# Kernel optimization log

Hardware: AMD Instinct MI355X
Metric: run time of the kernel (lower is better)

The kernel has to match this reference:

```python
import jax, jax.numpy as jnp
import numpy as np

B, S, DIM = 32, 1, 4096
HQ, HKV, HD = 32, 8, 128
MAX_SEQ = 2048
START_POS = 2047


def _apply_rope(t, cos, sin):
    # t: [B, S, H, HD]; cos/sin: [S, HD//2]; interleaved complex rotation (Llama style)
    b, s, h, d = t.shape
    t = t.reshape(b, s, h, d // 2, 2)
    t0, t1 = t[..., 0], t[..., 1]
    c = cos[None, :, None, :]
    sn = sin[None, :, None, :]
    out = jnp.stack([t0 * c - t1 * sn, t0 * sn + t1 * c], axis=-1)
    return out.reshape(b, s, h, d)


def setup_inputs() -> dict:
    key = jax.random.key(0)
    ks = jax.random.split(key, 8)
    w_scale = 0.02
    x = jax.random.normal(ks[0], (B, S, DIM), dtype=jnp.float32)
    wq = jax.random.normal(ks[1], (HQ * HD, DIM), dtype=jnp.float32) * w_scale
    wk = jax.random.normal(ks[2], (HKV * HD, DIM), dtype=jnp.float32) * w_scale
    wv = jax.random.normal(ks[3], (HKV * HD, DIM), dtype=jnp.float32) * w_scale
    wo = jax.random.normal(ks[4], (HQ * HD, DIM), dtype=jnp.float32).T * w_scale
    wo = jnp.asarray(wo)  # [DIM, HQ*HD] as torch Linear weight [out,in]
    cache_k = jax.random.normal(ks[5], (B, MAX_SEQ, HKV, HD), dtype=jnp.float32)
    cache_v = jax.random.normal(ks[6], (B, MAX_SEQ, HKV, HD), dtype=jnp.float32)
    # rotary frequencies for the current position(s)
    inv_freq = 1.0 / (10000.0 ** (np.arange(0, HD, 2, dtype=np.float32) / HD))  # [HD//2]
    pos = np.arange(START_POS, START_POS + S, dtype=np.float32)[:, None]  # [S,1]
    ang = pos * inv_freq[None, :]
    freqs_cos = jnp.asarray(np.cos(ang), dtype=jnp.float32)
    freqs_sin = jnp.asarray(np.sin(ang), dtype=jnp.float32)
    return {"x": x, "wq": wq, "wk": wk, "wv": wv, "wo": wo,
            "cache_k": cache_k, "cache_v": cache_v,
            "freqs_cos": freqs_cos, "freqs_sin": freqs_sin,
            "start_pos": START_POS}


def reference(x, wq, wk, wv, wo, cache_k, cache_v, freqs_cos, freqs_sin, start_pos):
    b, s, dim = x.shape
    hd = 2 * freqs_cos.shape[-1]
    hq = wq.shape[0] // hd
    hkv = wk.shape[0] // hd
    n_rep = hq // hkv

    # QKV projections (torch Linear: y = x @ W.T)
    xq = (x @ wq.T).reshape(b, s, hq, hd)
    xk = (x @ wk.T).reshape(b, s, hkv, hd)
    xv = (x @ wv.T).reshape(b, s, hkv, hd)

    # RoPE on q and k
    xq = _apply_rope(xq, freqs_cos, freqs_sin)
    xk = _apply_rope(xk, freqs_cos, freqs_sin)

    # KV cache update at start_pos (static python int -> static slicing)
    ck = jax.lax.dynamic_update_slice(cache_k, xk, (0, start_pos, 0, 0))
    cv = jax.lax.dynamic_update_slice(cache_v, xv, (0, start_pos, 0, 0))
    t = start_pos + s
    keys = ck[:, :t]    # [B, T, HKV, HD]
    values = cv[:, :t]  # [B, T, HKV, HD]

    # Grouped attention without materializing repeated KV (repeat_kv fused into einsum)
    q = xq.reshape(b, s, hkv, n_rep, hd)
    scores = jnp.einsum('bsgrd,btgd->bgrst', q, keys) / jnp.sqrt(jnp.asarray(hd, x.dtype))
    attn = jax.nn.softmax(scores, axis=-1)  # decode step: attends to full history, no mask
    out = jnp.einsum('bgrst,btgd->bsgrd', attn, values).reshape(b, s, hq * hd)
    return out @ wo.T  # [B, S, DIM]
```

## Files before the change

### kernel.cpp

```cpp
#include <hip/hip_runtime.h>
#include <hip/hip_bf16.h>

typedef float vf4 __attribute__((ext_vector_type(4)));

#define B_    32
#define DIM_  4096
#define TSEQ  2048
#define LASTT 2047
#define NCH   8
#define CHUNK 256
#define SCL   0.08838834764831845f
#define KS    16
#define KCH   256
#define ROWS1 6144
#define ROWS4 4096

__device__ __forceinline__ float dotv(vf4 a, vf4 b) {
    return fmaf(a[0], b[0], fmaf(a[1], b[1], fmaf(a[2], b[2], a[3] * b[3])));
}

__device__ __forceinline__ void gemm_tile_part(
    const float* __restrict__ W, const float* __restrict__ X,
    float* __restrict__ part, int rloc_base, int grow_base,
    int kb0, int kc, int rowsTot) {
    __shared__ __align__(16) vf4 wS[128][17];
    __shared__ __align__(16) vf4 xS[16][33];
    const int tid = threadIdx.x;
    const int rg = tid >> 3, bg = tid & 7;
    const int sr4 = tid >> 4, swf = tid & 15;
    const int sb = tid >> 3, sxf = tid & 7;
    float c[4][4] = {};

    for (int tile = 0; tile < 4; ++tile) {
        const int kb4 = (kb0 + tile * 64) >> 2;
        #pragma unroll
        for (int jj = 0; jj < 8; ++jj) {
            const int row = sr4 + 16 * jj;
            wS[row][swf] =
                ((const vf4*)(W + (size_t)(rloc_base + row) * DIM_))[kb4 + swf];
        }
        #pragma unroll
        for (int jj = 0; jj < 2; ++jj) {
            const int f4i = sxf + 8 * jj;
            xS[f4i][sb] = ((const vf4*)(X + (size_t)sb * DIM_))[kb4 + f4i];
        }
        __syncthreads();
        #pragma unroll
        for (int k4 = 0; k4 < 16; ++k4) {
            const vf4 w0 = wS[rg      ][k4];
            const vf4 w1 = wS[rg + 32 ][k4];
            const vf4 w2 = wS[rg + 64 ][k4];
            const vf4 w3 = wS[rg + 96 ][k4];
            const vf4 x0 = xS[k4][bg     ];
            const vf4 x1 = xS[k4][bg + 8 ];
            const vf4 x2 = xS[k4][bg + 16];
            const vf4 x3 = xS[k4][bg + 24];
            #pragma unroll
            for (int cm = 0; cm < 4; ++cm) {
                c[0][0] = fmaf(w0[cm], x0[cm], c[0][0]);
                c[0][1] = fmaf(w0[cm], x1[cm], c[0][1]);
                c[0][2] = fmaf(w0[cm], x2[cm], c[0][2]);
                c[0][3] = fmaf(w0[cm], x3[cm], c[0][3]);
                c[1][0] = fmaf(w1[cm], x0[cm], c[1][0]);
                c[1][1] = fmaf(w1[cm], x1[cm], c[1][1]);
                c[1][2] = fmaf(w1[cm], x2[cm], c[1][2]);
                c[1][3] = fmaf(w1[cm], x3[cm], c[1][3]);
                c[2][0] = fmaf(w2[cm], x0[cm], c[2][0]);
                c[2][1] = fmaf(w2[cm], x1[cm], c[2][1]);
                c[2][2] = fmaf(w2[cm], x2[cm], c[2][2]);
                c[2][3] = fmaf(w2[cm], x3[cm], c[2][3]);
                c[3][0] = fmaf(w3[cm], x0[cm], c[3][0]);
                c[3][1] = fmaf(w3[cm], x1[cm], c[3][1]);
                c[3][2] = fmaf(w3[cm], x2[cm], c[3][2]);
                c[3][3] = fmaf(w3[cm], x3[cm], c[3][3]);
            }
        }
        __syncthreads();
    }
    float* pb = part + (size_t)kc * rowsTot * 32;
    #pragma unroll
    for (int i = 0; i < 4; ++i)
        #pragma unroll
        for (int j = 0; j < 4; ++j)
            pb[(size_t)(grow_base + rg + 32 * i) * 32 + bg + 8 * j] = c[i][j];
}

__global__ __launch_bounds__(256) void k1_qkv(
    const float* __restrict__ x,  const float* __restrict__ wq,
    const float* __restrict__ wk, const float* __restrict__ wv,
    float* __restrict__ part) {
    const int rb = blockIdx.x >> 4, kc = blockIdx.x & 15;
    const int rbase = rb * 128;
    const float* W; int rloc;
    if (rbase < 4096)      { W = wq; rloc = rbase; }
    else if (rbase < 5120) { W = wk; rloc = rbase - 4096; }
    else                   { W = wv; rloc = rbase - 5120; }
    gemm_tile_part(W, x, part, rloc, rbase, kc * KCH, kc, ROWS1);
}

__global__ __launch_bounds__(256) void k1b_comb(
    const float* __restrict__ part, const float* __restrict__ fcos,
    const float* __restrict__ fsin, float* __restrict__ q_ws,
    float* __restrict__ k_ws, float* __restrict__ v_ws) {
    const int tid = threadIdx.x;
    const int b = tid & 31;
    const int row0 = (blockIdx.x * 8 + (tid >> 5)) * 2;
    float e = 0.f, o = 0.f;
    #pragma unroll
    for (int kc = 0; kc < 16; ++kc) {
        const float* pb = part + (size_t)kc * (ROWS1 * 32);
        e += pb[(size_t)row0 * 32 + b];
        o += pb[(size_t)(row0 + 1) * 32 + b];
    }
    if (row0 < 5120) {
        const int d = row0 & 127;
        const float cj = fcos[d >> 1], sj = fsin[d >> 1];
        const float re = e * cj - o * sj;
        const float ro = e * sj + o * cj;
        if (row0 < 4096) {
            q_ws[(size_t)b * 4096 + row0]     = re * SCL;
            q_ws[(size_t)b * 4096 + row0 + 1] = ro * SCL;
        } else {
            k_ws[(size_t)b * 1024 + row0 - 4096] = re;
            k_ws[(size_t)b * 1024 + row0 - 4095] = ro;
        }
    } else {
        v_ws[(size_t)b * 1024 + row0 - 5120] = e;
        v_ws[(size_t)b * 1024 + row0 - 5119] = o;
    }
}

__global__ __launch_bounds__(256) void k2_attn(
    const float* __restrict__ q_ws, const float* __restrict__ k_ws,
    const float* __restrict__ v_ws, const float* __restrict__ cK,
    const float* __restrict__ cV,   float* __restrict__ cws) {
    __shared__ __align__(16) float p_lds[4][260];
    __shared__ __align__(16) float pacc[4][4][128];
    __shared__ float wred[4][4];
    __shared__ float wsum[4][4];
    const int blk = blockIdx.x;
    const int b = blk >> 6, g = (blk >> 3) & 7, c = blk & 7;
    const int tid = threadIdx.x, wave = tid >> 6, lane = tid & 63;
    const int tbase = c * CHUNK + wave * 64;
    const int s = lane & 7, pown = lane >> 3;

    const vf4* qb4 = (const vf4*)(q_ws + ((size_t)b * 32 + g * 4) * 128);
    vf4 q4[4][4];
    #pragma unroll
    for (int r = 0; r < 4; ++r)
        #pragma unroll
        for (int j = 0; j < 4; ++j)
            q4[r][j] = qb4[r * 32 + j * 8 + s];

    const vf4* kwsrow = (const vf4*)(k_ws + ((size_t)b * 8 + g) * 128);
    const vf4* vwsrow = (const vf4*)(v_ws + ((size_t)b * 8 + g) * 128);

    vf4 kb[4];
    {
        const int t = tbase + pown;
        const vf4* kr = (t == LASTT) ? kwsrow
            : (const vf4*)(cK + (((size_t)b * TSEQ + t) * 8 + g) * 128);
        #pragma unroll
        for (int j = 0; j < 4; ++j)
            kb[j] = __builtin_nontemporal_load(&kr[j * 8 + s]);
    }
    #pragma unroll
    for (int pg = 0; pg < 8; ++pg) {
        vf4 kn[4];
        if (pg < 7) {
            const int t = tbase + (pg + 1) * 8 + pown;
            const vf4* kr = (t == LASTT) ? kwsrow
                : (const vf4*)(cK + (((size_t)b * TSEQ + t) * 8 + g) * 128);
            #pragma unroll
            for (int j = 0; j < 4; ++j)
                kn[j] = __builtin_nontemporal_load(&kr[j * 8 + s]);
        }
        float a0 = 0.f, a1 = 0.f, a2 = 0.f, a3 = 0.f;
        #pragma unroll
        for (int j = 0; j < 4; ++j) {
            a0 += dotv(q4[0][j], kb[j]);
            a1 += dotv(q4[1][j], kb[j]);
            a2 += dotv(q4[2][j], kb[j]);
            a3 += dotv(q4[3][j], kb[j]);
        }
        #pragma unroll
        for (int m = 4; m >= 1; m >>= 1) {
            a0 += __shfl_xor(a0, m); a1 += __shfl_xor(a1, m);
            a2 += __shfl_xor(a2, m); a3 += __shfl_xor(a3, m);
        }
        const int idx = wave * 64 + pg * 8 + pown;
        if (s == 0) p_lds[0][idx] = a0;
        if (s == 1) p_lds[1][idx] = a1;
        if (s == 2) p_lds[2][idx] = a2;
        if (s == 3) p_lds[3][idx] = a3;
        #pragma unroll
        for (int j = 0; j < 4; ++j) kb[j] = kn[j];
    }

    float sc[4];
    #pragma unroll
    for (int r = 0; r < 4; ++r) sc[r] = p_lds[r][wave * 64 + lane];
    #pragma unroll
    for (int r = 0; r < 4; ++r) {
        float m = sc[r];
        #pragma unroll
        for (int msk = 32; msk >= 1; msk >>= 1) m = fmaxf(m, __shfl_xor(m, msk));
        if (lane == 0) wred[wave][r] = m;
    }
    __syncthreads();
    float M[4], S[4];
    #pragma unroll
    for (int r = 0; r < 4; ++r)
        M[r] = fmaxf(fmaxf(wred[0][r], wred[1][r]), fmaxf(wred[2][r], wred[3][r]));
    #pragma unroll
    for (int r = 0; r < 4; ++r) {
        const float p = __expf(sc[r] - M[r]);
        p_lds[r][wave * 64 + lane] = p;
        float su = p;
        #pragma unroll
        for (int msk = 32; msk >= 1; msk >>= 1) su += __shfl_xor(su, msk);
        if (lane == 0) wsum[wave][r] = su;
    }
    __syncthreads();
    #pragma unroll
    for (int r = 0; r < 4; ++r)
        S[r] = wsum[0][r] + wsum[1][r] + wsum[2][r] + wsum[3][r];

    const int h = lane >> 5, col = lane & 31;
    float a[4][4] = {};
    #pragma unroll
    for (int tt = 0; tt < 8; ++tt) {
        vf4 vv[4];
        #pragma unroll
        for (int u = 0; u < 4; ++u) {
            const int t = tbase + tt * 8 + u * 2 + h;
            const vf4* vp = (t == LASTT) ? vwsrow
                : (const vf4*)(cV + (((size_t)b * TSEQ + t) * 8 + g) * 128);
            vv[u] = __builtin_nontemporal_load(&vp[col]);
        }
        #pragma unroll
        for (int u = 0; u < 4; ++u) {
            #pragma unroll
            for (int r = 0; r < 4; ++r) {
                const float pr = p_lds[r][wave * 64 + tt * 8 + u * 2 + h];
                a[r][0] = fmaf(pr, vv[u][0], a[r][0]);
                a[r][1] = fmaf(pr, vv[u][1], a[r][1]);
                a[r][2] = fmaf(pr, vv[u][2], a[r][2]);
                a[r][3] = fmaf(pr, vv[u][3], a[r][3]);
            }
        }
    }
    #pragma unroll
    for (int r = 0; r < 4; ++r)
        #pragma unroll
        for (int j = 0; j < 4; ++j) a[r][j] += __shfl_xor(a[r][j], 32);
    if (lane < 32) {
        #pragma unroll
        for (int r = 0; r < 4; ++r) {
            vf4 v; v[0] = a[r][0]; v[1] = a[r][1]; v[2] = a[r][2]; v[3] = a[r][3];
            *(vf4*)&pacc[wave][r][col * 4] = v;
        }
    }
    __syncthreads();
    const size_t base = (size_t)blk * 520;
    for (int o = tid; o < 512; o += 256) {
        const int r = o >> 7, d = o & 127;
        cws[base + r * 130 + d] =
            pacc[0][r][d] + pacc[1][r][d] + pacc[2][r][d] + pacc[3][r][d];
    }
    if (tid == 0) {
        #pragma unroll
        for (int r = 0; r < 4; ++r) {
            cws[base + r * 130 + 128] = M[r];
            cws[base + r * 130 + 129] = S[r];
        }
    }
}

__global__ __launch_bounds__(256) void k3_comb(const float* __restrict__ cws,
                                               float* __restrict__ attn) {
    const int blk = blockIdx.x;
    const int b = blk >> 3, g = blk & 7;
    const int tid = threadIdx.x, r = tid >> 6, lane = tid & 63;
    const size_t base0 = (size_t)blk * 8 * 520 + r * 130;
    float mi[8], si[8];
    float Mg = -3.4e38f;
    #pragma unroll
    for (int ci = 0; ci < 8; ++ci) {
        mi[ci] = cws[base0 + (size_t)ci * 520 + 128];
        si[ci] = cws[base0 + (size_t)ci * 520 + 129];
        Mg = fmaxf(Mg, mi[ci]);
    }
    float w[8], Sg = 0.f;
    #pragma unroll
    for (int ci = 0; ci < 8; ++ci) {
        w[ci] = __expf(mi[ci] - Mg);
        Sg = fmaf(si[ci], w[ci], Sg);
    }
    const float inv = 1.f / Sg;
    #pragma unroll
    for (int dd = 0; dd < 2; ++dd) {
        const int d = lane + dd * 64;
        float o = 0.f;
        #pragma unroll
        for (int ci = 0; ci < 8; ++ci)
            o = fmaf(cws[base0 + (size_t)ci * 520 + d], w[ci], o);
        attn[((size_t)b * 32 + g * 4 + r) * 128 + d] = o * inv;
    }
}

__global__ __launch_bounds__(256) void k4_out(
    const float* __restrict__ attn, const float* __restrict__ wo,
    float* __restrict__ part) {
    const int rb = blockIdx.x >> 4, kc = blockIdx.x & 15;
    const int rbase = rb * 128;
    gemm_tile_part(wo, attn, part, rbase, rbase, kc * KCH, kc, ROWS4);
}

__global__ __launch_bounds__(256) void k4b_comb(const float* __restrict__ part,
                                                float* __restrict__ out) {
    const int tid = threadIdx.x;
    const int b = tid & 31;
    const int row = blockIdx.x * 8 + (tid >> 5);
    float acc = 0.f;
    #pragma unroll
    for (int kc = 0; kc < 16; ++kc)
        acc += part[(size_t)kc * (ROWS4 * 32) + (size_t)row * 32 + b];
    out[(size_t)b * 4096 + row] = acc;
}

extern "C" void kernel_launch(void* const* d_in, const int* in_sizes, int n_in,
                              void* d_out, int out_size, void* d_ws, size_t ws_size,
                              hipStream_t stream) {
    const float* x    = (const float*)d_in[0];
    const float* wq   = (const float*)d_in[1];
    const float* wk   = (const float*)d_in[2];
    const float* wv   = (const float*)d_in[3];
    const float* wo   = (const float*)d_in[4];
    const float* cK   = (const float*)d_in[5];
    const float* cV   = (const float*)d_in[6];
    const float* fcos = (const float*)d_in[7];
    const float* fsin = (const float*)d_in[8];
    float* ws   = (float*)d_ws;
    float* A    = ws;
    float* q_ws = ws + 3145728;
    float* k_ws = ws + 3276800;
    float* v_ws = ws + 3309568;
    float* attn = ws + 3342336;
    float* out  = (float*)d_out;

    hipLaunchKernelGGL(k1_qkv,   dim3(768),  dim3(256), 0, stream,
                       x, wq, wk, wv, A);
    hipLaunchKernelGGL(k1b_comb, dim3(384),  dim3(256), 0, stream,
                       A, fcos, fsin, q_ws, k_ws, v_ws);
    hipLaunchKernelGGL(k2_attn,  dim3(2048), dim3(256), 0, stream,
                       q_ws, k_ws, v_ws, cK, cV, A);
    hipLaunchKernelGGL(k3_comb,  dim3(256),  dim3(256), 0, stream, A, attn);
    hipLaunchKernelGGL(k4_out,   dim3(512),  dim3(256), 0, stream, attn, wo, A);
    hipLaunchKernelGGL(k4b_comb, dim3(512),  dim3(256), 0, stream, A, out);
}
```

Baseline: 160.7 us.

## Replace split-K partial buffers with atomic reductions and prefetch V in attention

The QKV and output GEMMs now accumulate their split-K partial sums straight into zeroed destination buffers with float atomicAdd. RoPE moves into the GEMM epilogue, using a lane shuffle to pair even and odd rows. This removes the two combine kernels and the round trip of the partial buffer through memory, at the cost of two memsets, atomic contention and non-deterministic summation order. The attention kernel also software-pipelines the V-cache loads one step ahead, and weight loads become nontemporal.

```diff
diff --git a/kernel.cpp b/kernel.cpp
--- a/kernel.cpp
+++ b/kernel.cpp
@@ -10,34 +10,29 @@
 #define NCH   8
 #define CHUNK 256
 #define SCL   0.08838834764831845f
-#define KS    16
 #define KCH   256
-#define ROWS1 6144
-#define ROWS4 4096
 
 __device__ __forceinline__ float dotv(vf4 a, vf4 b) {
     return fmaf(a[0], b[0], fmaf(a[1], b[1], fmaf(a[2], b[2], a[3] * b[3])));
 }
 
-__device__ __forceinline__ void gemm_tile_part(
+__device__ __forceinline__ void gemm_tile(
     const float* __restrict__ W, const float* __restrict__ X,
-    float* __restrict__ part, int rloc_base, int grow_base,
-    int kb0, int kc, int rowsTot) {
+    int kb0, float c[4][4]) {
     __shared__ __align__(16) vf4 wS[128][17];
     __shared__ __align__(16) vf4 xS[16][33];
     const int tid = threadIdx.x;
     const int rg = tid >> 3, bg = tid & 7;
     const int sr4 = tid >> 4, swf = tid & 15;
     const int sb = tid >> 3, sxf = tid & 7;
-    float c[4][4] = {};
 
     for (int tile = 0; tile < 4; ++tile) {
         const int kb4 = (kb0 + tile * 64) >> 2;
         #pragma unroll
         for (int jj = 0; jj < 8; ++jj) {
             const int row = sr4 + 16 * jj;
-            wS[row][swf] =
-                ((const vf4*)(W + (size_t)(rloc_base + row) * DIM_))[kb4 + swf];
+            wS[row][swf] = __builtin_nontemporal_load(
+                ((const vf4*)(W + (size_t)row * DIM_)) + kb4 + swf);
         }
         #pragma unroll
         for (int jj = 0; jj < 2; ++jj) {
@@ -77,56 +72,47 @@
         }
         __syncthreads();
     }
-    float* pb = part + (size_t)kc * rowsTot * 32;
-    #pragma unroll
-    for (int i = 0; i < 4; ++i)
-        #pragma unroll
-        for (int j = 0; j < 4; ++j)
-            pb[(size_t)(grow_base + rg + 32 * i) * 32 + bg + 8 * j] = c[i][j];
 }
 
 __global__ __launch_bounds__(256) void k1_qkv(
     const float* __restrict__ x,  const float* __restrict__ wq,
     const float* __restrict__ wk, const float* __restrict__ wv,
-    float* __restrict__ part) {
+    const float* __restrict__ fcos, const float* __restrict__ fsin,
+    float* __restrict__ q_ws, float* __restrict__ k_ws, float* __restrict__ v_ws) {
     const int rb = blockIdx.x >> 4, kc = blockIdx.x & 15;
     const int rbase = rb * 128;
-    const float* W; int rloc;
-    if (rbase < 4096)      { W = wq; rloc = rbase; }
-    else if (rbase < 5120) { W = wk; rloc = rbase - 4096; }
-    else                   { W = wv; rloc = rbase - 5120; }
-    gemm_tile_part(W, x, part, rloc, rbase, kc * KCH, kc, ROWS1);
-}
-
-__global__ __launch_bounds__(256) void k1b_comb(
-    const float* __restrict__ part, const float* __restrict__ fcos,
-    const float* __restrict__ fsin, float* __restrict__ q_ws,
-    float* __restrict__ k_ws, float* __restrict__ v_ws) {
+    const float* W; int rloc, kind;
+    if (rbase < 4096)      { W = wq; rloc = rbase;        kind = 0; }
+    else if (rbase < 5120) { W = wk; rloc = rbase - 4096; kind = 1; }
+    else                   { W = wv; rloc = rbase - 5120; kind = 2; }
+    float c[4][4] = {};
+    gemm_tile(W + (size_t)rloc * DIM_, x, kc * KCH, c);
+
     const int tid = threadIdx.x;
-    const int b = tid & 31;
-    const int row0 = (blockIdx.x * 8 + (tid >> 5)) * 2;
-    float e = 0.f, o = 0.f;
-    #pragma unroll
-    for (int kc = 0; kc < 16; ++kc) {
-        const float* pb = part + (size_t)kc * (ROWS1 * 32);
-        e += pb[(size_t)row0 * 32 + b];
-        o += pb[(size_t)(row0 + 1) * 32 + b];
-    }
-    if (row0 < 5120) {
-        const int d = row0 & 127;
-        const float cj = fcos[d >> 1], sj = fsin[d >> 1];
-        const float re = e * cj - o * sj;
-        const float ro = e * sj + o * cj;
-        if (row0 < 4096) {
-            q_ws[(size_t)b * 4096 + row0]     = re * SCL;
-            q_ws[(size_t)b * 4096 + row0 + 1] = ro * SCL;
-        } else {
-            k_ws[(size_t)b * 1024 + row0 - 4096] = re;
-            k_ws[(size_t)b * 1024 + row0 - 4095] = ro;
-        }
-    } else {
-        v_ws[(size_t)b * 1024 + row0 - 5120] = e;
-        v_ws[(size_t)b * 1024 + row0 - 5119] = o;
+    const int rg = tid >> 3, bg = tid & 7;
+    float* dst = (kind == 0) ? q_ws : (kind == 1 ? k_ws : v_ws);
+    const int stride = (kind == 0) ? 4096 : 1024;
+    #pragma unroll
+    for (int i = 0; i < 4; ++i) {
+        const int row = rloc + rg + 32 * i;
+        float vals[4];
+        #pragma unroll
+        for (int j = 0; j < 4; ++j) vals[j] = c[i][j];
+        if (kind <= 1) {
+            const int pi = (row & 126) >> 1;
+            const float cj = fcos[pi], sj = fsin[pi];
+            #pragma unroll
+            for (int j = 0; j < 4; ++j) {
+                const float partner = __shfl_xor(vals[j], 8);
+                float v = ((rg & 1) == 0) ? (vals[j] * cj - partner * sj)
+                                          : (partner * sj + vals[j] * cj);
+                if (kind == 0) v *= SCL;
+                vals[j] = v;
+            }
+        }
+        #pragma unroll
+        for (int j = 0; j < 4; ++j)
+            atomicAdd(&dst[(size_t)(bg + 8 * j) * stride + row], vals[j]);
     }
 }
 
@@ -197,6 +183,16 @@
         for (int j = 0; j < 4; ++j) kb[j] = kn[j];
     }
 
+    const int h = lane >> 5, col = lane & 31;
+    vf4 vb[4];
+    #pragma unroll
+    for (int u = 0; u < 4; ++u) {
+        const int t = tbase + u * 2 + h;
+        const vf4* vp = (t == LASTT) ? vwsrow
+            : (const vf4*)(cV + (((size_t)b * TSEQ + t) * 8 + g) * 128);
+        vb[u] = __builtin_nontemporal_load(&vp[col]);
+    }
+
     float sc[4];
     #pragma unroll
     for (int r = 0; r < 4; ++r) sc[r] = p_lds[r][wave * 64 + lane];
@@ -226,29 +222,32 @@
     for (int r = 0; r < 4; ++r)
         S[r] = wsum[0][r] + wsum[1][r] + wsum[2][r] + wsum[3][r];
 
-    const int h = lane >> 5, col = lane & 31;
     float a[4][4] = {};
     #pragma unroll
     for (int tt = 0; tt < 8; ++tt) {
-        vf4 vv[4];
-        #pragma unroll
-        for (int u = 0; u < 4; ++u) {
-            const int t = tbase + tt * 8 + u * 2 + h;
-            const vf4* vp = (t == LASTT) ? vwsrow
-                : (const vf4*)(cV + (((size_t)b * TSEQ + t) * 8 + g) * 128);
-            vv[u] = __builtin_nontemporal_load(&vp[col]);
+        vf4 vn[4];
+        if (tt < 7) {
+            #pragma unroll
+            for (int u = 0; u < 4; ++u) {
+                const int t = tbase + (tt + 1) * 8 + u * 2 + h;
+                const vf4* vp = (t == LASTT) ? vwsrow
+                    : (const vf4*)(cV + (((size_t)b * TSEQ + t) * 8 + g) * 128);
+                vn[u] = __builtin_nontemporal_load(&vp[col]);
+            }
         }
         #pragma unroll
         for (int u = 0; u < 4; ++u) {
             #pragma unroll
             for (int r = 0; r < 4; ++r) {
                 const float pr = p_lds[r][wave * 64 + tt * 8 + u * 2 + h];
-                a[r][0] = fmaf(pr, vv[u][0], a[r][0]);
-                a[r][1] = fmaf(pr, vv[u][1], a[r][1]);
-                a[r][2] = fmaf(pr, vv[u][2], a[r][2]);
-                a[r][3] = fmaf(pr, vv[u][3], a[r][3]);
+                a[r][0] = fmaf(pr, vb[u][0], a[r][0]);
+                a[r][1] = fmaf(pr, vb[u][1], a[r][1]);
+                a[r][2] = fmaf(pr, vb[u][2], a[r][2]);
+                a[r][3] = fmaf(pr, vb[u][3], a[r][3]);
             }
         }
+        #pragma unroll
+        for (int u = 0; u < 4; ++u) vb[u] = vn[u];
     }
     #pragma unroll
     for (int r = 0; r < 4; ++r)
@@ -311,22 +310,20 @@
 
 __global__ __launch_bounds__(256) void k4_out(
     const float* __restrict__ attn, const float* __restrict__ wo,
-    float* __restrict__ part) {
+    float* __restrict__ out) {
     const int rb = blockIdx.x >> 4, kc = blockIdx.x & 15;
     const int rbase = rb * 128;
-    gemm_tile_part(wo, attn, part, rbase, rbase, kc * KCH, kc, ROWS4);
-}
-
-__global__ __launch_bounds__(256) void k4b_comb(const float* __restrict__ part,
-                                                float* __restrict__ out) {
+    float c[4][4] = {};
+    gemm_tile(wo + (size_t)rbase * DIM_, attn, kc * KCH, c);
     const int tid = threadIdx.x;
-    const int b = tid & 31;
-    const int row = blockIdx.x * 8 + (tid >> 5);
-    float acc = 0.f;
-    #pragma unroll
-    for (int kc = 0; kc < 16; ++kc)
-        acc += part[(size_t)kc * (ROWS4 * 32) + (size_t)row * 32 + b];
-    out[(size_t)b * 4096 + row] = acc;
+    const int rg = tid >> 3, bg = tid & 7;
+    #pragma unroll
+    for (int i = 0; i < 4; ++i) {
+        const int row = rbase + rg + 32 * i;
+        #pragma unroll
+        for (int j = 0; j < 4; ++j)
+            atomicAdd(&out[(size_t)(bg + 8 * j) * 4096 + row], c[i][j]);
+    }
 }
 
 extern "C" void kernel_launch(void* const* d_in, const int* in_sizes, int n_in,
@@ -342,20 +339,19 @@
     const float* fcos = (const float*)d_in[7];
     const float* fsin = (const float*)d_in[8];
     float* ws   = (float*)d_ws;
-    float* A    = ws;
-    float* q_ws = ws + 3145728;
-    float* k_ws = ws + 3276800;
-    float* v_ws = ws + 3309568;
-    float* attn = ws + 3342336;
+    float* q_ws = ws;
+    float* k_ws = ws + 131072;
+    float* v_ws = ws + 163840;
+    float* cws  = ws + 196608;
+    float* attn = ws + 1261568;
     float* out  = (float*)d_out;
 
-    hipLaunchKernelGGL(k1_qkv,   dim3(768),  dim3(256), 0, stream,
-                       x, wq, wk, wv, A);
-    hipLaunchKernelGGL(k1b_comb, dim3(384),  dim3(256), 0, stream,
-                       A, fcos, fsin, q_ws, k_ws, v_ws);
-    hipLaunchKernelGGL(k2_attn,  dim3(2048), dim3(256), 0, stream,
-                       q_ws, k_ws, v_ws, cK, cV, A);
-    hipLaunchKernelGGL(k3_comb,  dim3(256),  dim3(256), 0, stream, A, attn);
-    hipLaunchKernelGGL(k4_out,   dim3(512),  dim3(256), 0, stream, attn, wo, A);
-    hipLaunchKernelGGL(k4b_comb, dim3(512),  dim3(256), 0, stream, A, out);
-}
+    hipMemsetAsync(q_ws, 0, 196608 * sizeof(float), stream);
+    hipMemsetAsync(out,  0, (size_t)out_size * sizeof(float), stream);
+    hipLaunchKernelGGL(k1_qkv,  dim3(768),  dim3(256), 0, stream,
+                       x, wq, wk, wv, fcos, fsin, q_ws, k_ws, v_ws);
+    hipLaunchKernelGGL(k2_attn, dim3(2048), dim3(256), 0, stream,
+                       q_ws, k_ws, v_ws, cK, cV, cws);
+    hipLaunchKernelGGL(k3_comb, dim3(256),  dim3(256), 0, stream, cws, attn);
+    hipLaunchKernelGGL(k4_out,  dim3(512),  dim3(256), 0, stream, attn, wo, out);
+}
```

Result: slower. 196.4 us (+22.2%).

## Split attention into single-wave 64-token chunks and pipeline V loads

Applied to the files above, without the earlier changes.

The attention kernel changes from 256-thread blocks over 256-token chunks to 64-thread, single-wave blocks over 64-token chunks (8192 blocks). This removes the cross-wave LDS reductions and most barriers, and each block writes its partial result directly. The PV loop now prefetches the next V row one step ahead, and the combine kernel merges 32 partials instead of 8, which means more workspace traffic. Weight tiles in the GEMM are also loaded with nontemporal hints.

```diff
diff --git a/kernel.cpp b/kernel.cpp
--- a/kernel.cpp
+++ b/kernel.cpp
@@ -7,10 +7,11 @@
 #define DIM_  4096
 #define TSEQ  2048
 #define LASTT 2047
-#define NCH   8
-#define CHUNK 256
+#define NCH   32
+#define CHUNK 64
+#define CSTR  528
+#define RSTR  132
 #define SCL   0.08838834764831845f
-#define KS    16
 #define KCH   256
 #define ROWS1 6144
 #define ROWS4 4096
@@ -36,8 +37,8 @@
         #pragma unroll
         for (int jj = 0; jj < 8; ++jj) {
             const int row = sr4 + 16 * jj;
-            wS[row][swf] =
-                ((const vf4*)(W + (size_t)(rloc_base + row) * DIM_))[kb4 + swf];
+            wS[row][swf] = __builtin_nontemporal_load(
+                ((const vf4*)(W + (size_t)(rloc_base + row) * DIM_)) + kb4 + swf);
         }
         #pragma unroll
         for (int jj = 0; jj < 2; ++jj) {
@@ -130,18 +131,15 @@
     }
 }
 
-__global__ __launch_bounds__(256) void k2_attn(
+__global__ __launch_bounds__(64) void k2_attn(
     const float* __restrict__ q_ws, const float* __restrict__ k_ws,
     const float* __restrict__ v_ws, const float* __restrict__ cK,
     const float* __restrict__ cV,   float* __restrict__ cws) {
-    __shared__ __align__(16) float p_lds[4][260];
-    __shared__ __align__(16) float pacc[4][4][128];
-    __shared__ float wred[4][4];
-    __shared__ float wsum[4][4];
+    __shared__ float p_lds[4][64];
     const int blk = blockIdx.x;
-    const int b = blk >> 6, g = (blk >> 3) & 7, c = blk & 7;
-    const int tid = threadIdx.x, wave = tid >> 6, lane = tid & 63;
-    const int tbase = c * CHUNK + wave * 64;
+    const int b = blk >> 8, g = (blk >> 5) & 7, c = blk & 31;
+    const int lane = threadIdx.x & 63;
+    const int tbase = c * CHUNK;
     const int s = lane & 7, pown = lane >> 3;
 
     const vf4* qb4 = (const vf4*)(q_ws + ((size_t)b * 32 + g * 4) * 128);
@@ -188,7 +186,7 @@
             a0 += __shfl_xor(a0, m); a1 += __shfl_xor(a1, m);
             a2 += __shfl_xor(a2, m); a3 += __shfl_xor(a3, m);
         }
-        const int idx = wave * 64 + pg * 8 + pown;
+        const int idx = pg * 8 + pown;
         if (s == 0) p_lds[0][idx] = a0;
         if (s == 1) p_lds[1][idx] = a1;
         if (s == 2) p_lds[2][idx] = a2;
@@ -196,83 +194,73 @@
         #pragma unroll
         for (int j = 0; j < 4; ++j) kb[j] = kn[j];
     }
-
-    float sc[4];
-    #pragma unroll
-    for (int r = 0; r < 4; ++r) sc[r] = p_lds[r][wave * 64 + lane];
+    __syncthreads();
+
+    const int h = lane >> 5, col = lane & 31;
+    vf4 vb;
+    {
+        const int t = tbase + h;
+        const vf4* vp = (t == LASTT) ? vwsrow
+            : (const vf4*)(cV + (((size_t)b * TSEQ + t) * 8 + g) * 128);
+        vb = __builtin_nontemporal_load(&vp[col]);
+    }
+
+    float sc[4], M[4], S[4];
+    #pragma unroll
+    for (int r = 0; r < 4; ++r) sc[r] = p_lds[r][lane];
     #pragma unroll
     for (int r = 0; r < 4; ++r) {
         float m = sc[r];
         #pragma unroll
         for (int msk = 32; msk >= 1; msk >>= 1) m = fmaxf(m, __shfl_xor(m, msk));
-        if (lane == 0) wred[wave][r] = m;
+        M[r] = m;
+        const float p = __expf(sc[r] - m);
+        p_lds[r][lane] = p;
+        float su = p;
+        #pragma unroll
+        for (int msk = 32; msk >= 1; msk >>= 1) su += __shfl_xor(su, msk);
+        S[r] = su;
     }
     __syncthreads();
-    float M[4], S[4];
-    #pragma unroll
-    for (int r = 0; r < 4; ++r)
-        M[r] = fmaxf(fmaxf(wred[0][r], wred[1][r]), fmaxf(wred[2][r], wred[3][r]));
-    #pragma unroll
-    for (int r = 0; r < 4; ++r) {
-        const float p = __expf(sc[r] - M[r]);
-        p_lds[r][wave * 64 + lane] = p;
-        float su = p;
-        #pragma unroll
-        for (int msk = 32; msk >= 1; msk >>= 1) su += __shfl_xor(su, msk);
-        if (lane == 0) wsum[wave][r] = su;
-    }
-    __syncthreads();
-    #pragma unroll
-    for (int r = 0; r < 4; ++r)
-        S[r] = wsum[0][r] + wsum[1][r] + wsum[2][r] + wsum[3][r];
-
-    const int h = lane >> 5, col = lane & 31;
+
     float a[4][4] = {};
-    #pragma unroll
-    for (int tt = 0; tt < 8; ++tt) {
-        vf4 vv[4];
-        #pragma unroll
-        for (int u = 0; u < 4; ++u) {
-            const int t = tbase + tt * 8 + u * 2 + h;
+    #pragma unroll 8
+    for (int tt = 0; tt < 32; ++tt) {
+        vf4 vn;
+        if (tt < 31) {
+            const int t = tbase + (tt + 1) * 2 + h;
             const vf4* vp = (t == LASTT) ? vwsrow
                 : (const vf4*)(cV + (((size_t)b * TSEQ + t) * 8 + g) * 128);
-            vv[u] = __builtin_nontemporal_load(&vp[col]);
-        }
-        #pragma unroll
-        for (int u = 0; u < 4; ++u) {
-            #pragma unroll
-            for (int r = 0; r < 4; ++r) {
-                const float pr = p_lds[r][wave * 64 + tt * 8 + u * 2 + h];
-                a[r][0] = fmaf(pr, vv[u][0], a[r][0]);
-                a[r][1] = fmaf(pr, vv[u][1], a[r][1]);
-                a[r][2] = fmaf(pr, vv[u][2], a[r][2]);
-                a[r][3] = fmaf(pr, vv[u][3], a[r][3]);
-            }
-        }
+            vn = __builtin_nontemporal_load(&vp[col]);
+        }
+        #pragma unroll
+        for (int r = 0; r < 4; ++r) {
+            const float pr = p_lds[r][tt * 2 + h];
+            a[r][0] = fmaf(pr, vb[0], a[r][0]);
+            a[r][1] = fmaf(pr, vb[1], a[r][1]);
+            a[r][2] = fmaf(pr, vb[2], a[r][2]);
+            a[r][3] = fmaf(pr, vb[3], a[r][3]);
+        }
+        vb = vn;
     }
     #pragma unroll
     for (int r = 0; r < 4; ++r)
         #pragma unroll
         for (int j = 0; j < 4; ++j) a[r][j] += __shfl_xor(a[r][j], 32);
+
+    float* base = cws + (size_t)blk * CSTR;
     if (lane < 32) {
         #pragma unroll
         for (int r = 0; r < 4; ++r) {
             vf4 v; v[0] = a[r][0]; v[1] = a[r][1]; v[2] = a[r][2]; v[3] = a[r][3];
-            *(vf4*)&pacc[wave][r][col * 4] = v;
-        }
-    }
-    __syncthreads();
-    const size_t base = (size_t)blk * 520;
-    for (int o = tid; o < 512; o += 256) {
-        const int r = o >> 7, d = o & 127;
-        cws[base + r * 130 + d] =
-            pacc[0][r][d] + pacc[1][r][d] + pacc[2][r][d] + pacc[3][r][d];
-    }
-    if (tid == 0) {
+            *(vf4*)(base + r * RSTR + col * 4) = v;
+        }
+    }
+    if (lane == 0) {
         #pragma unroll
         for (int r = 0; r < 4; ++r) {
-            cws[base + r * 130 + 128] = M[r];
-            cws[base + r * 130 + 129] = S[r];
+            base[r * RSTR + 128] = M[r];
+            base[r * RSTR + 129] = S[r];
         }
     }
 }
@@ -282,18 +270,18 @@
     const int blk = blockIdx.x;
     const int b = blk >> 3, g = blk & 7;
     const int tid = threadIdx.x, r = tid >> 6, lane = tid & 63;
-    const size_t base0 = (size_t)blk * 8 * 520 + r * 130;
-    float mi[8], si[8];
+    const float* base0 = cws + (size_t)blk * 32 * CSTR + r * RSTR;
+    float mi[32], si[32];
     float Mg = -3.4e38f;
     #pragma unroll
-    for (int ci = 0; ci < 8; ++ci) {
-        mi[ci] = cws[base0 + (size_t)ci * 520 + 128];
-        si[ci] = cws[base0 + (size_t)ci * 520 + 129];
+    for (int ci = 0; ci < 32; ++ci) {
+        mi[ci] = base0[(size_t)ci * CSTR + 128];
+        si[ci] = base0[(size_t)ci * CSTR + 129];
         Mg = fmaxf(Mg, mi[ci]);
     }
-    float w[8], Sg = 0.f;
-    #pragma unroll
-    for (int ci = 0; ci < 8; ++ci) {
+    float w[32], Sg = 0.f;
+    #pragma unroll
+    for (int ci = 0; ci < 32; ++ci) {
         w[ci] = __expf(mi[ci] - Mg);
         Sg = fmaf(si[ci], w[ci], Sg);
     }
@@ -303,8 +291,8 @@
         const int d = lane + dd * 64;
         float o = 0.f;
         #pragma unroll
-        for (int ci = 0; ci < 8; ++ci)
-            o = fmaf(cws[base0 + (size_t)ci * 520 + d], w[ci], o);
+        for (int ci = 0; ci < 32; ++ci)
+            o = fmaf(base0[(size_t)ci * CSTR + d], w[ci], o);
         attn[((size_t)b * 32 + g * 4 + r) * 128 + d] = o * inv;
     }
 }
@@ -343,17 +331,17 @@
     const float* fsin = (const float*)d_in[8];
     float* ws   = (float*)d_ws;
     float* A    = ws;
-    float* q_ws = ws + 3145728;
-    float* k_ws = ws + 3276800;
-    float* v_ws = ws + 3309568;
-    float* attn = ws + 3342336;
+    float* q_ws = ws + 4325376;
+    float* k_ws = ws + 4456448;
+    float* v_ws = ws + 4489216;
+    float* attn = ws + 4521984;
     float* out  = (float*)d_out;
 
     hipLaunchKernelGGL(k1_qkv,   dim3(768),  dim3(256), 0, stream,
                        x, wq, wk, wv, A);
     hipLaunchKernelGGL(k1b_comb, dim3(384),  dim3(256), 0, stream,
                        A, fcos, fsin, q_ws, k_ws, v_ws);
-    hipLaunchKernelGGL(k2_attn,  dim3(2048), dim3(256), 0, stream,
+    hipLaunchKernelGGL(k2_attn,  dim3(8192), dim3(64),  0, stream,
                        q_ws, k_ws, v_ws, cK, cV, A);
     hipLaunchKernelGGL(k3_comb,  dim3(256),  dim3(256), 0, stream, A, attn);
     hipLaunchKernelGGL(k4_out,   dim3(512),  dim3(256), 0, stream, attn, wo, A);
```

Result: slower. 186.8 us (+16.2%).
